# Performance work log

Hardware: AMD Instinct MI355X
Metric: run time of the kernel (lower is better)

Reference implementation:

```python
import jax, jax.numpy as jnp
import numpy as np

L = 2000          # per-modality dialogue length (all_dia_len)
M = 3             # num_modal
F = 512           # feature_size
E = 400000        # number of edges (<= 500000 edge_weight params)
N = M * L         # total nodes
NUM_LAYERS = 2
EW_SIZE = 500000
W_SCALE = 0.044   # ~1/sqrt(F) to keep activations sane


def setup_inputs() -> dict:
    key = jax.random.key(0)
    ks = jax.random.split(key, 9)
    x_a = jax.random.normal(ks[0], (L, F), jnp.float32)
    x_v = jax.random.normal(ks[1], (L, F), jnp.float32)
    x_t = jax.random.normal(ks[2], (L, F), jnp.float32)
    edge_index = jax.random.randint(ks[3], (2, E), 0, N, dtype=jnp.int32)
    edge_weight_param = jnp.ones((EW_SIZE,), jnp.float32)
    gcn_W = jax.random.normal(ks[4], (NUM_LAYERS, F, F), jnp.float32) * W_SCALE
    gcn_b = jnp.zeros((NUM_LAYERS, F), jnp.float32)
    fc_W = jax.random.normal(ks[5], (NUM_LAYERS, F, F), jnp.float32) * W_SCALE
    fc_b = jnp.zeros((NUM_LAYERS, F), jnp.float32)
    return {
        "x_a": x_a, "x_v": x_v, "x_t": x_t,
        "edge_weight_param": edge_weight_param,
        "gcn_W": gcn_W, "gcn_b": gcn_b,
        "fc_W": fc_W, "fc_b": fc_b,
        "edge_index": edge_index,
    }


def _gcn_fact(edge_index, edge_weight, num_nodes):
    # sparse edge list -> dense adjacency (scatter-add, duplicate edges coalesce)
    adj = jnp.zeros((num_nodes, num_nodes), edge_weight.dtype)
    adj = adj.at[edge_index[0], edge_index[1]].add(edge_weight)
    row_sum = adj.sum(axis=1)
    # torch: pow(row_sum, -0.5), inf -> 0  (safe form for zero-degree nodes)
    pos = row_sum > 0
    d_inv_sqrt = jnp.where(pos, jax.lax.rsqrt(jnp.where(pos, row_sum, 1.0)), 0.0)
    # D^{-1/2} A D^{-1/2} via row/col broadcast (same math as diag matmuls)
    return d_inv_sqrt[:, None] * adj * d_inv_sqrt[None, :]


def reference(x_a, x_v, x_t, edge_weight_param, gcn_W, gcn_b, fc_W, fc_b, edge_index):
    feature = jnp.concatenate([x_a, x_v, x_t], axis=0)      # [N, F]
    edge_weight = edge_weight_param[: edge_index.shape[1]]   # [E]
    gcn = _gcn_fact(edge_index, edge_weight, feature.shape[0])
    feature_sum = feature
    for i in range(NUM_LAYERS):
        # encoder layer: one dense GCN propagation + projection
        feature = jax.nn.relu(gcn @ feature @ gcn_W[i] + gcn_b[i])
        # fc layer: Linear + LeakyReLU (dropout = identity at eval)
        feature_sum = feature_sum + jax.nn.leaky_relu(feature @ fc_W[i] + fc_b[i], 0.01)
    # chunk back into per-modality features
    return tuple(jnp.split(feature_sum, M, axis=0))
```

## Files before the change

### kernel.cpp

```cpp
#include <hip/hip_runtime.h>
#include <hip/hip_bf16.h>

#define LL 2000
#define MM 3
#define FF 512
#define NN (MM * LL)
#define CAP 128

typedef __attribute__((ext_vector_type(8))) short bf16x8;
typedef __attribute__((ext_vector_type(4))) float f32x4;

__device__ __forceinline__ unsigned short f2bf(float x) {
    __hip_bfloat16 b = __float2bfloat16(x);
    return *(unsigned short*)&b;
}

__device__ __forceinline__ void gload16(const void* gsrc, void* ldst) {
    __builtin_amdgcn_global_load_lds((const __attribute__((address_space(1))) unsigned int*)gsrc,
                                     (__attribute__((address_space(3))) unsigned int*)ldst,
                                     16, 0, 0);
}

__global__ __launch_bounds__(256) void prep(const float* __restrict__ xa,
                                            const float* __restrict__ xv,
                                            const float* __restrict__ xt,
                                            unsigned short* __restrict__ feat,
                                            float* __restrict__ out_sum,
                                            const float* __restrict__ gcnW,
                                            const float* __restrict__ fcW,
                                            unsigned short* __restrict__ Wt,
                                            const int* __restrict__ esrc,
                                            int* __restrict__ counts,
                                            int* __restrict__ pir, int E) {
    __shared__ unsigned short tile[64][65];
    int b = blockIdx.x;
    int tid = threadIdx.x;
    if (b < 3000) {
        int idx4 = b * 256 + tid;
        const int per4 = (LL * FF) / 4;
        const float4* src;
        int off;
        if (idx4 < per4)            { src = (const float4*)xa; off = idx4; }
        else if (idx4 < 2 * per4)   { src = (const float4*)xv; off = idx4 - per4; }
        else                        { src = (const float4*)xt; off = idx4 - 2 * per4; }
        float4 v = src[off];
        ((float4*)out_sum)[idx4] = v;
        ushort4 pk;
        pk.x = f2bf(v.x); pk.y = f2bf(v.y); pk.z = f2bf(v.z); pk.w = f2bf(v.w);
        ((ushort4*)feat)[idx4] = pk;
    } else if (b < 3256) {
        int idx = b - 3000;
        int mz = idx >> 6;
        int rem = idx & 63;
        int k0 = (rem >> 3) * 64;
        int n0 = (rem & 7) * 64;
        int layer = (mz < 2) ? mz : mz - 2;
        const float* src = (mz < 2) ? (gcnW + (size_t)layer * FF * FF)
                                    : (fcW + (size_t)layer * FF * FF);
        int slot = (mz < 2) ? (mz * 2) : ((mz - 2) * 2 + 1);
        unsigned short* dst = Wt + (size_t)slot * FF * FF;
        for (int i = tid; i < 64 * 64; i += 256) {
            int r = i >> 6, c = i & 63;
            tile[r][c] = f2bf(src[(size_t)(k0 + r) * FF + n0 + c]);
        }
        __syncthreads();
        for (int i = tid; i < 64 * 64; i += 256) {
            int r = i >> 6, c = i & 63;
            dst[(size_t)(n0 + r) * FF + k0 + c] = tile[c][r];
        }
    } else {
        int e = (b - 3256) * 256 + tid;
        if (e < E) pir[e] = atomicAdd(&counts[esrc[e]], 1);
    }
}

__global__ __launch_bounds__(256) void gemm0_scatter(const unsigned short* __restrict__ A,
                                                     const unsigned short* __restrict__ Bt,
                                                     unsigned short* __restrict__ Hout,
                                                     int M, int gxm, int sblk,
                                                     const int* __restrict__ esrc,
                                                     const int* __restrict__ edst,
                                                     const float* __restrict__ ew,
                                                     const int* __restrict__ pir,
                                                     unsigned int* __restrict__ bucket, int E) {
    __shared__ short As[64 * 64];
    __shared__ short Bs[64 * 64];
    int b = blockIdx.x;
    int tid = threadIdx.x;
    if (b < sblk) {
        int e = b * 256 + tid;
        if (e < E) {
            int r = esrc[e];
            int slot = pir[e];
            if (slot < CAP)
                bucket[(size_t)r * CAP + slot] =
                    ((unsigned int)f2bf(ew[e]) << 16) | (unsigned int)edst[e];
        }
        return;
    }
    int bg = b - sblk;
    int wave = tid >> 6;
    int lane = tid & 63;
    int lane16 = lane & 15;
    int quad = lane >> 4;
    int m0 = (bg % gxm) * 64;
    int n0 = (bg / gxm) * 64;
    int wm = (wave >> 1) * 32;
    int wn = (wave & 1) * 32;

    f32x4 acc[2][2] = {};

    for (int k0 = 0; k0 < FF; k0 += 64) {
#pragma unroll
        for (int s = 0; s < 2; s++) {
            int c = wave * 128 + s * 64 + lane;
            int row = c >> 3;
            int kc = (c & 7) ^ (row & 7);
            int ar = m0 + row; if (ar >= M) ar = M - 1;
            gload16((const short*)A + (size_t)ar * FF + k0 + kc * 8,
                    &As[(wave * 128 + s * 64) * 8]);
            gload16((const short*)Bt + (size_t)(n0 + row) * FF + k0 + kc * 8,
                    &Bs[(wave * 128 + s * 64) * 8]);
        }
        __syncthreads();
#pragma unroll
        for (int kk = 0; kk < 2; kk++) {
            bf16x8 a[2], bb[2];
#pragma unroll
            for (int mt = 0; mt < 2; mt++) {
                int row = wm + mt * 16 + lane16;
                int kc = (kk * 4 + quad) ^ (row & 7);
                a[mt] = *(const bf16x8*)&As[row * 64 + kc * 8];
            }
#pragma unroll
            for (int nt = 0; nt < 2; nt++) {
                int row = wn + nt * 16 + lane16;
                int kc = (kk * 4 + quad) ^ (row & 7);
                bb[nt] = *(const bf16x8*)&Bs[row * 64 + kc * 8];
            }
#pragma unroll
            for (int mt = 0; mt < 2; mt++)
#pragma unroll
                for (int nt = 0; nt < 2; nt++)
                    acc[mt][nt] = __builtin_amdgcn_mfma_f32_16x16x32_bf16(a[mt], bb[nt], acc[mt][nt], 0, 0, 0);
        }
        __syncthreads();
    }

#pragma unroll
    for (int mt = 0; mt < 2; mt++) {
#pragma unroll
        for (int nt = 0; nt < 2; nt++) {
            int n = n0 + wn + nt * 16 + lane16;
#pragma unroll
            for (int rr = 0; rr < 4; rr++) {
                int m = m0 + wm + mt * 16 + quad * 4 + rr;
                if (m < M) Hout[(size_t)m * FF + n] = f2bf(acc[mt][nt][rr]);
            }
        }
    }
}

__global__ __launch_bounds__(256) void rowsum_dinv(const unsigned int* __restrict__ bucket,
                                                   const int* __restrict__ counts,
                                                   float* __restrict__ dinv) {
    int wave = threadIdx.x >> 6, lane = threadIdx.x & 63;
    int r = blockIdx.x * 4 + wave;
    int s = r * CAP;
    int e = s + min(counts[r], CAP);
    float sum = 0.0f;
    for (int i = s + lane; i < e; i += 64)
        sum += __uint_as_float(bucket[i] & 0xFFFF0000u);
#pragma unroll
    for (int off = 32; off > 0; off >>= 1) sum += __shfl_xor(sum, off);
    if (lane == 0) dinv[r] = (sum > 0.0f) ? rsqrtf(sum) : 0.0f;
}

__device__ __forceinline__ void accum8(float* acc, uint4 h, float v) {
    unsigned int d[4] = {h.x, h.y, h.z, h.w};
#pragma unroll
    for (int k = 0; k < 4; k++) {
        float lo = __uint_as_float(d[k] << 16);
        float hi = __uint_as_float(d[k] & 0xFFFF0000u);
        acc[2 * k]     = fmaf(v, lo, acc[2 * k]);
        acc[2 * k + 1] = fmaf(v, hi, acc[2 * k + 1]);
    }
}

__global__ __launch_bounds__(256) void spmm_bias_relu(const unsigned short* __restrict__ H,
                                                      const int* __restrict__ counts,
                                                      const unsigned int* __restrict__ bucket,
                                                      const float* __restrict__ dinv,
                                                      const float* __restrict__ bias,
                                                      unsigned short* __restrict__ featOut) {
    int wave = threadIdx.x >> 6, lane = threadIdx.x & 63;
    int r = blockIdx.x * 4 + wave;
    int s = r * CAP;
    int e = s + min(counts[r], CAP);
    int f0 = lane * 8;
    const unsigned short* Hf = H + f0;
    float acc[8] = {0, 0, 0, 0, 0, 0, 0, 0};

    int i = s;
    uint4 pk;
    bool have = (i + 4 <= e);
    if (have) pk = *(const uint4*)&bucket[i];
    while (have) {
        unsigned int q0 = pk.x, q1 = pk.y, q2 = pk.z, q3 = pk.w;
        uint4 a0 = *(const uint4*)(Hf + (size_t)(q0 & 0xFFFF) * FF);
        uint4 a1 = *(const uint4*)(Hf + (size_t)(q1 & 0xFFFF) * FF);
        uint4 a2 = *(const uint4*)(Hf + (size_t)(q2 & 0xFFFF) * FF);
        uint4 a3 = *(const uint4*)(Hf + (size_t)(q3 & 0xFFFF) * FF);
        float v0 = __uint_as_float(q0 & 0xFFFF0000u) * dinv[q0 & 0xFFFF];
        float v1 = __uint_as_float(q1 & 0xFFFF0000u) * dinv[q1 & 0xFFFF];
        float v2 = __uint_as_float(q2 & 0xFFFF0000u) * dinv[q2 & 0xFFFF];
        float v3 = __uint_as_float(q3 & 0xFFFF0000u) * dinv[q3 & 0xFFFF];
        i += 4;
        have = (i + 4 <= e);
        if (have) pk = *(const uint4*)&bucket[i];
        accum8(acc, a0, v0);
        accum8(acc, a1, v1);
        accum8(acc, a2, v2);
        accum8(acc, a3, v3);
    }
    for (; i < e; i++) {
        unsigned int q = bucket[i];
        uint4 a = *(const uint4*)(Hf + (size_t)(q & 0xFFFF) * FF);
        accum8(acc, a, __uint_as_float(q & 0xFFFF0000u) * dinv[q & 0xFFFF]);
    }

    float dr = dinv[r];
    float4 b0 = *(const float4*)(bias + f0);
    float4 b1 = *(const float4*)(bias + f0 + 4);
    float bb[8] = {b0.x, b0.y, b0.z, b0.w, b1.x, b1.y, b1.z, b1.w};
    unsigned int o[4];
#pragma unroll
    for (int k = 0; k < 4; k++) {
        float v0 = fmaxf(fmaf(acc[2 * k], dr, bb[2 * k]), 0.0f);
        float v1 = fmaxf(fmaf(acc[2 * k + 1], dr, bb[2 * k + 1]), 0.0f);
        o[k] = (unsigned int)f2bf(v0) | ((unsigned int)f2bf(v1) << 16);
    }
    uint4 ov; ov.x = o[0]; ov.y = o[1]; ov.z = o[2]; ov.w = o[3];
    *(uint4*)(featOut + (size_t)r * FF + f0) = ov;
}

template <int MODE>
__global__ __launch_bounds__(256) void gemm_bf16(const unsigned short* __restrict__ A,
                                                 const unsigned short* __restrict__ Bt,
                                                 const float* __restrict__ fbias,
                                                 unsigned short* __restrict__ Hout,
                                                 float* __restrict__ out,
                                                 int M) {
    __shared__ short As[64 * 64];
    __shared__ short Bs[64 * 64];
    int tid = threadIdx.x;
    int wave = tid >> 6;
    int lane = tid & 63;
    int lane16 = lane & 15;
    int quad = lane >> 4;
    int m0 = blockIdx.x * 64;
    int n0 = blockIdx.y * 64;
    int wm = (wave >> 1) * 32;
    int wn = (wave & 1) * 32;

    f32x4 acc[2][2] = {};

    for (int k0 = 0; k0 < FF; k0 += 64) {
#pragma unroll
        for (int s = 0; s < 2; s++) {
            int c = wave * 128 + s * 64 + lane;
            int row = c >> 3;
            int kc = (c & 7) ^ (row & 7);
            int ar = m0 + row; if (ar >= M) ar = M - 1;
            gload16((const short*)A + (size_t)ar * FF + k0 + kc * 8,
                    &As[(wave * 128 + s * 64) * 8]);
            gload16((const short*)Bt + (size_t)(n0 + row) * FF + k0 + kc * 8,
                    &Bs[(wave * 128 + s * 64) * 8]);
        }
        __syncthreads();
#pragma unroll
        for (int kk = 0; kk < 2; kk++) {
            bf16x8 a[2], bb[2];
#pragma unroll
            for (int mt = 0; mt < 2; mt++) {
                int row = wm + mt * 16 + lane16;
                int kc = (kk * 4 + quad) ^ (row & 7);
                a[mt] = *(const bf16x8*)&As[row * 64 + kc * 8];
            }
#pragma unroll
            for (int nt = 0; nt < 2; nt++) {
                int row = wn + nt * 16 + lane16;
                int kc = (kk * 4 + quad) ^ (row & 7);
                bb[nt] = *(const bf16x8*)&Bs[row * 64 + kc * 8];
            }
#pragma unroll
            for (int mt = 0; mt < 2; mt++)
#pragma unroll
                for (int nt = 0; nt < 2; nt++)
                    acc[mt][nt] = __builtin_amdgcn_mfma_f32_16x16x32_bf16(a[mt], bb[nt], acc[mt][nt], 0, 0, 0);
        }
        __syncthreads();
    }

    bool isFc = (MODE == 1) || (MODE == 2 && n0 < FF);
#pragma unroll
    for (int mt = 0; mt < 2; mt++) {
#pragma unroll
        for (int nt = 0; nt < 2; nt++) {
            int n = n0 + wn + nt * 16 + lane16;
            float bv = isFc ? fbias[n] : 0.0f;
#pragma unroll
            for (int rr = 0; rr < 4; rr++) {
                int m = m0 + wm + mt * 16 + quad * 4 + rr;
                if (m < M) {
                    float v = acc[mt][nt][rr];
                    if (isFc) {
                        v += bv;
                        v = (v > 0.0f) ? v : 0.01f * v;
                        out[(size_t)m * FF + n] += v;
                    } else {
                        Hout[(size_t)m * FF + (n - FF)] = f2bf(v);
                    }
                }
            }
        }
    }
}

extern "C" void kernel_launch(void* const* d_in, const int* in_sizes, int n_in,
                              void* d_out, int out_size, void* d_ws, size_t ws_size,
                              hipStream_t stream) {
    const float* xa      = (const float*)d_in[0];
    const float* xv      = (const float*)d_in[1];
    const float* xt      = (const float*)d_in[2];
    const float* ew      = (const float*)d_in[3];
    const float* gcn_W   = (const float*)d_in[4];
    const float* gcn_b   = (const float*)d_in[5];
    const float* fc_W    = (const float*)d_in[6];
    const float* fc_b    = (const float*)d_in[7];
    const int*   eidx    = (const int*)d_in[8];
    const int E = in_sizes[8] / 2;
    const int* esrc = eidx;
    const int* edst = eidx + E;

    float* out = (float*)d_out;

    char* w = (char*)d_ws;
    int*          counts = (int*)         (w + 0);
    float*        dinv   = (float*)       (w + 24064);
    unsigned int* bucket = (unsigned int*)(w + 48128);
    unsigned short* feat = (unsigned short*)(w + 3120128);
    unsigned short* H    = (unsigned short*)(w + 9264128);
    unsigned short* Wt   = (unsigned short*)(w + 15408128);
    int*          pir    = (int*)         (w + 17505280);

    hipMemsetAsync(counts, 0, 24000, stream);

    const int eblocks = (E + 255) / 256;
    prep<<<3256 + eblocks, 256, 0, stream>>>(xa, xv, xt, feat, out,
                                             gcn_W, fc_W, Wt, esrc, counts, pir, E);

    const int gxm = (NN + 63) / 64;
    const int ngemm0 = gxm * 8;
    gemm0_scatter<<<eblocks + ngemm0, 256, 0, stream>>>(feat, Wt, H, NN, gxm, eblocks,
                                                        esrc, edst, ew, pir, bucket, E);
    rowsum_dinv<<<NN / 4, 256, 0, stream>>>(bucket, counts, dinv);

    spmm_bias_relu<<<NN / 4, 256, 0, stream>>>(H, counts, bucket, dinv, gcn_b, feat);
    gemm_bf16<2><<<dim3(gxm, 16), 256, 0, stream>>>(feat, Wt + (size_t)FF * FF, fc_b, H, out, NN);
    spmm_bias_relu<<<NN / 4, 256, 0, stream>>>(H, counts, bucket, dinv, gcn_b + FF, feat);
    gemm_bf16<1><<<dim3(gxm, 8), 256, 0, stream>>>(feat, Wt + (size_t)3 * FF * FF, fc_b + FF, nullptr, out, NN);
}
```

Measured before the change: 210.6 us.

## Fuse edge bucketing and float rowsum into prep, fold dinv into gemm0

The edge pass in prep now claims a bucket slot with an atomic counter, writes the packed bf16 weight and destination directly, and atomically accumulates an fp32 row sum. The separate scatter blocks, the pir array and the rowsum_dinv kernel are removed, and dinv is computed from the fp32 row sums by extra blocks in the first GEMM launch. This saves one launch and a round trip over the edge arrays and bucket. In exchange it adds float atomics on row sums and makes the degree use fp32 rather than bf16-truncated weights, so edges beyond CAP now count toward the degree.

After: 230.0 us. 9.2% more time.

```diff
diff --git a/kernel.cpp b/kernel.cpp
--- a/kernel.cpp
+++ b/kernel.cpp
@@ -30,8 +30,11 @@
                                             const float* __restrict__ fcW,
                                             unsigned short* __restrict__ Wt,
                                             const int* __restrict__ esrc,
+                                            const int* __restrict__ edst,
+                                            const float* __restrict__ ew,
                                             int* __restrict__ counts,
-                                            int* __restrict__ pir, int E) {
+                                            float* __restrict__ rowsumF,
+                                            unsigned int* __restrict__ bucket, int E) {
     __shared__ unsigned short tile[64][65];
     int b = blockIdx.x;
     int tid = threadIdx.x;
@@ -70,35 +73,38 @@
         }
     } else {
         int e = (b - 3256) * 256 + tid;
-        if (e < E) pir[e] = atomicAdd(&counts[esrc[e]], 1);
-    }
-}
-
-__global__ __launch_bounds__(256) void gemm0_scatter(const unsigned short* __restrict__ A,
-                                                     const unsigned short* __restrict__ Bt,
-                                                     unsigned short* __restrict__ Hout,
-                                                     int M, int gxm, int sblk,
-                                                     const int* __restrict__ esrc,
-                                                     const int* __restrict__ edst,
-                                                     const float* __restrict__ ew,
-                                                     const int* __restrict__ pir,
-                                                     unsigned int* __restrict__ bucket, int E) {
+        if (e < E) {
+            int r = esrc[e];
+            float wv = ew[e];
+            int slot = atomicAdd(&counts[r], 1);
+            if (slot < CAP)
+                bucket[(size_t)r * CAP + slot] =
+                    ((unsigned int)f2bf(wv) << 16) | (unsigned int)edst[e];
+            atomicAdd(&rowsumF[r], wv);
+        }
+    }
+}
+
+#define DINV_BLK 24
+__global__ __launch_bounds__(256) void gemm0_dinv(const unsigned short* __restrict__ A,
+                                                  const unsigned short* __restrict__ Bt,
+                                                  unsigned short* __restrict__ Hout,
+                                                  int M, int gxm,
+                                                  const float* __restrict__ rowsumF,
+                                                  float* __restrict__ dinv) {
     __shared__ short As[64 * 64];
     __shared__ short Bs[64 * 64];
     int b = blockIdx.x;
     int tid = threadIdx.x;
-    if (b < sblk) {
-        int e = b * 256 + tid;
-        if (e < E) {
-            int r = esrc[e];
-            int slot = pir[e];
-            if (slot < CAP)
-                bucket[(size_t)r * CAP + slot] =
-                    ((unsigned int)f2bf(ew[e]) << 16) | (unsigned int)edst[e];
+    if (b < DINV_BLK) {
+        int i = b * 256 + tid;
+        if (i < NN) {
+            float s = rowsumF[i];
+            dinv[i] = (s > 0.0f) ? rsqrtf(s) : 0.0f;
         }
         return;
     }
-    int bg = b - sblk;
+    int bg = b - DINV_BLK;
     int wave = tid >> 6;
     int lane = tid & 63;
     int lane16 = lane & 15;
@@ -159,21 +165,6 @@
             }
         }
     }
-}
-
-__global__ __launch_bounds__(256) void rowsum_dinv(const unsigned int* __restrict__ bucket,
-                                                   const int* __restrict__ counts,
-                                                   float* __restrict__ dinv) {
-    int wave = threadIdx.x >> 6, lane = threadIdx.x & 63;
-    int r = blockIdx.x * 4 + wave;
-    int s = r * CAP;
-    int e = s + min(counts[r], CAP);
-    float sum = 0.0f;
-    for (int i = s + lane; i < e; i += 64)
-        sum += __uint_as_float(bucket[i] & 0xFFFF0000u);
-#pragma unroll
-    for (int off = 32; off > 0; off >>= 1) sum += __shfl_xor(sum, off);
-    if (lane == 0) dinv[r] = (sum > 0.0f) ? rsqrtf(sum) : 0.0f;
 }
 
 __device__ __forceinline__ void accum8(float* acc, uint4 h, float v) {
@@ -346,25 +337,24 @@
     float* out = (float*)d_out;
 
     char* w = (char*)d_ws;
-    int*          counts = (int*)         (w + 0);
-    float*        dinv   = (float*)       (w + 24064);
-    unsigned int* bucket = (unsigned int*)(w + 48128);
-    unsigned short* feat = (unsigned short*)(w + 3120128);
-    unsigned short* H    = (unsigned short*)(w + 9264128);
-    unsigned short* Wt   = (unsigned short*)(w + 15408128);
-    int*          pir    = (int*)         (w + 17505280);
-
-    hipMemsetAsync(counts, 0, 24000, stream);
+    int*          counts  = (int*)         (w + 0);
+    float*        rowsumF = (float*)       (w + 24064);
+    float*        dinv    = (float*)       (w + 48128);
+    unsigned int* bucket  = (unsigned int*)(w + 72192);
+    unsigned short* feat  = (unsigned short*)(w + 3144192);
+    unsigned short* H     = (unsigned short*)(w + 9288192);
+    unsigned short* Wt    = (unsigned short*)(w + 15432192);
+
+    hipMemsetAsync(counts, 0, 48128, stream);
 
     const int eblocks = (E + 255) / 256;
     prep<<<3256 + eblocks, 256, 0, stream>>>(xa, xv, xt, feat, out,
-                                             gcn_W, fc_W, Wt, esrc, counts, pir, E);
+                                             gcn_W, fc_W, Wt, esrc, edst, ew,
+                                             counts, rowsumF, bucket, E);
 
     const int gxm = (NN + 63) / 64;
     const int ngemm0 = gxm * 8;
-    gemm0_scatter<<<eblocks + ngemm0, 256, 0, stream>>>(feat, Wt, H, NN, gxm, eblocks,
-                                                        esrc, edst, ew, pir, bucket, E);
-    rowsum_dinv<<<NN / 4, 256, 0, stream>>>(bucket, counts, dinv);
+    gemm0_dinv<<<DINV_BLK + ngemm0, 256, 0, stream>>>(feat, Wt, H, NN, gxm, rowsumF, dinv);
 
     spmm_bias_relu<<<NN / 4, 256, 0, stream>>>(H, counts, bucket, dinv, gcn_b, feat);
     gemm_bf16<2><<<dim3(gxm, 16), 256, 0, stream>>>(feat, Wt + (size_t)FF * FF, fc_b, H, out, NN);
```
